# Optimization experiments

Measured on AMD Instinct MI355X. Metric: run time of the kernel, lower is better.

## Reference

```python
import jax, jax.numpy as jnp
import numpy as np

# static config (levels=4, CDA=False branch -> self_attn_4, scale=4, f=False)
SHAPES = [(80, 80), (40, 40), (20, 20), (10, 10)]
D = 256; NH = 8; NL = 4; NP = 4; DFF = 1024; DH = D // NH
L = sum(h * w for h, w in SHAPES)  # 8500
B = 1


def layer_norm(x, g, b, eps=1e-5):
    m = jnp.mean(x, axis=-1, keepdims=True)
    v = jnp.mean((x - m) ** 2, axis=-1, keepdims=True)
    return (x - m) * jax.lax.rsqrt(v + eps) * g + b


def ms_deform_attn_core(value, loc, attn):
    # value: [B, L, NH, DH]; loc: [B, Lq, NH, NL, NP, 2] in [0,1]; attn: [B, Lq, NH, NL, NP]
    Bq, Lq = loc.shape[0], loc.shape[1]
    out = jnp.zeros((Bq, NH, Lq, DH), value.dtype)
    start = 0
    for lvl, (Hl, Wl) in enumerate(SHAPES):
        v = value[:, start:start + Hl * Wl]          # [B, HW, NH, DH]
        start += Hl * Wl
        v = v.transpose(0, 2, 1, 3)                  # [B, NH, HW, DH]
        ll = loc[:, :, :, lvl]                       # [B, Lq, NH, NP, 2]
        # grid_sample semantics: align_corners=False, padding_mode='zeros'
        x = ll[..., 0] * Wl - 0.5
        y = ll[..., 1] * Hl - 0.5
        x0 = jnp.floor(x); y0 = jnp.floor(y)
        acc = jnp.zeros((Bq, NH, Lq, NP, DH), value.dtype)
        for dy in (0, 1):
            for dx in (0, 1):
                xi = x0 + dx; yi = y0 + dy
                w = (1.0 - jnp.abs(x - xi)) * (1.0 - jnp.abs(y - yi))  # [B,Lq,NH,NP]
                valid = (xi >= 0) & (xi < Wl) & (yi >= 0) & (yi < Hl)
                xi_c = jnp.clip(xi, 0, Wl - 1).astype(jnp.int32)
                yi_c = jnp.clip(yi, 0, Hl - 1).astype(jnp.int32)
                lin = (yi_c * Wl + xi_c).transpose(0, 2, 1, 3).reshape(Bq, NH, Lq * NP)
                g = jnp.take_along_axis(v, lin[..., None], axis=2).reshape(Bq, NH, Lq, NP, DH)
                wv = (w * valid.astype(w.dtype)).transpose(0, 2, 1, 3)[..., None]
                acc = acc + g * wv
        aw = attn[:, :, :, lvl].transpose(0, 2, 1, 3)[..., None]  # [B,NH,Lq,NP,1]
        out = out + jnp.sum(acc * aw, axis=3)
    return out.transpose(0, 2, 1, 3).reshape(Bq, Lq, NH * DH)


def setup_inputs():
    key = jax.random.key(0)
    ks = jax.random.split(key, 24)
    s = 0.02
    d = {}
    d['src'] = jax.random.normal(ks[0], (B, L, D), jnp.float32)
    d['pos'] = jax.random.normal(ks[1], (B, L, D), jnp.float32)
    d['reference_points'] = jax.random.uniform(ks[2], (B, L, NL, 2), jnp.float32)
    d['spatial_shapes'] = jnp.array(SHAPES, jnp.int32)
    d['level_start_index'] = jnp.array(np.cumsum([0] + [h * w for h, w in SHAPES[:-1]]), jnp.int32)
    d['scale'] = 4
    # MSDeformAttn params
    d['Wo'] = jax.random.normal(ks[3], (D, NH * NL * NP * 2), jnp.float32) * s
    d['bo'] = jax.random.normal(ks[4], (NH * NL * NP * 2,), jnp.float32) * s
    d['Wa'] = jax.random.normal(ks[5], (D, NH * NL * NP), jnp.float32) * s
    d['ba'] = jax.random.normal(ks[6], (NH * NL * NP,), jnp.float32) * s
    d['Wv'] = jax.random.normal(ks[7], (D, D), jnp.float32) * s
    d['bv'] = jnp.zeros((D,), jnp.float32)
    d['Wout'] = jax.random.normal(ks[8], (D, D), jnp.float32) * s
    d['bout'] = jnp.zeros((D,), jnp.float32)
    # FFN + LayerNorms
    d['W1'] = jax.random.normal(ks[9], (D, DFF), jnp.float32) * s
    d['b1'] = jnp.zeros((DFF,), jnp.float32)
    d['W2'] = jax.random.normal(ks[10], (DFF, D), jnp.float32) * s
    d['b2'] = jnp.zeros((D,), jnp.float32)
    d['g1'] = jnp.ones((D,), jnp.float32); d['be1'] = jnp.zeros((D,), jnp.float32)
    d['g2'] = jnp.ones((D,), jnp.float32); d['be2'] = jnp.zeros((D,), jnp.float32)
    return d


def reference(src, pos, reference_points, spatial_shapes, level_start_index, scale,
              Wo, bo, Wa, ba, Wv, bv, Wout, bout, W1, b1, W2, b2, g1, be1, g2, be2):
    Bq, Lq, _ = src.shape
    q = src + pos  # with_pos_embed
    # sampling offsets & attention weights (softmax over levels*points)
    off = (q @ Wo + bo).reshape(Bq, Lq, NH, NL, NP, 2)
    attn = jax.nn.softmax((q @ Wa + ba).reshape(Bq, Lq, NH, NL * NP), axis=-1)
    attn = attn.reshape(Bq, Lq, NH, NL, NP)
    value = (src @ Wv + bv).reshape(Bq, L, NH, DH)
    # offset normalizer is (W, H) per level
    normalizer = jnp.stack([spatial_shapes[:, 1], spatial_shapes[:, 0]], -1).astype(src.dtype)
    loc = reference_points[:, :, None, :, None, :] + off / normalizer[None, None, None, :, None, :]
    src2 = ms_deform_attn_core(value, loc, attn) @ Wout + bout
    # residual + norm1 (dropout = eval identity)
    x = layer_norm(src + src2, g1, be1)
    # FFN
    ffn = jax.nn.relu(x @ W1 + b1) @ W2 + b2
    x = layer_norm(x + ffn, g2, be2)
    return x
```

## Files before the change

### kernel.cpp

```cpp
#include <hip/hip_runtime.h>
#include <hip/hip_bf16.h>
#include <string.h>

#define D 256
#define NH 8
#define DH 32
#define NL 4
#define NP 4
#define DFF 1024
#define LTOT 8500

typedef __bf16 bf16x8 __attribute__((ext_vector_type(8)));
typedef float floatx4 __attribute__((ext_vector_type(4)));

__device__ inline unsigned bpack(float a, float b) {
    __hip_bfloat16 ha = __float2bfloat16(a), hb = __float2bfloat16(b);
    unsigned short ua, ub;
    memcpy(&ua, &ha, 2); memcpy(&ub, &hb, 2);
    return (unsigned)ua | ((unsigned)ub << 16);
}

__global__ void transpose_all(const float* W0, const float* W1_, const float* W2_,
                              const float* W3, const float* W4, const float* W5,
                              __hip_bfloat16* T0, __hip_bfloat16* T1, __hip_bfloat16* T2,
                              __hip_bfloat16* T3, __hip_bfloat16* T4, __hip_bfloat16* T5) {
    const int cum[7] = {0, 64, 96, 160, 224, 480, 736};
    int id = blockIdx.x;
    int mi = 0;
    while (id >= cum[mi + 1]) mi++;
    int lid = id - cum[mi];
    const float* W; __hip_bfloat16* T; int K, N;
    switch (mi) {
        case 0: W = W0; T = T0; K = 256;  N = 256;  break;
        case 1: W = W1_; T = T1; K = 256; N = 128;  break;
        case 2: W = W2_; T = T2; K = 256; N = 256;  break;
        case 3: W = W3; T = T3; K = 256;  N = 256;  break;
        case 4: W = W4; T = T4; K = 256;  N = 1024; break;
        default: W = W5; T = T5; K = 1024; N = 256; break;
    }
    int ntx = N >> 5;
    int n0 = (lid % ntx) * 32, k0 = (lid / ntx) * 32;
    __shared__ float t[32][33];
    int tx = threadIdx.x & 31, ty = threadIdx.x >> 5;
#pragma unroll
    for (int i = 0; i < 32; i += 8)
        t[ty + i][tx] = W[(size_t)(k0 + ty + i) * N + n0 + tx];
    __syncthreads();
#pragma unroll
    for (int i = 0; i < 32; i += 8)
        T[(size_t)(n0 + ty + i) * K + k0 + tx] = __float2bfloat16(t[tx][ty + i]);
}

template<int BM, int BN>
__global__ __launch_bounds__(256) void gemm_mfma(
    const __hip_bfloat16* __restrict__ A, const __hip_bfloat16* __restrict__ BT,
    const float* __restrict__ bias, float* __restrict__ Cf, __hip_bfloat16* __restrict__ Cb,
    int M, int N, int K, int relu) {
    constexpr int BK = 32;
    constexpr int LDA = BK + 8;
    __shared__ __align__(16) __hip_bfloat16 sA[BM * LDA];
    __shared__ __align__(16) __hip_bfloat16 sB[BN * LDA];

    int tid = threadIdx.x;
    int wave = tid >> 6, lane = tid & 63;
    int m0 = blockIdx.y * BM;
    int n0 = blockIdx.x * BN;
    constexpr int WM = BM / 2, WN = BN / 2;
    int wm = (wave >> 1) * WM;
    int wn = (wave & 1) * WN;
    constexpr int TM = WM / 16, TN = WN / 16;

    floatx4 acc[TM][TN];
#pragma unroll
    for (int i = 0; i < TM; i++)
#pragma unroll
        for (int j = 0; j < TN; j++)
#pragma unroll
            for (int e = 0; e < 4; e++) acc[i][j][e] = 0.f;

    constexpr int RA = BM / 64, RB = BN / 64;
    int rowT = tid >> 2;
    int c16 = tid & 3;
    int lrow = lane & 15;
    int lk = (lane >> 4) * 8;

    int growA[RA];
#pragma unroll
    for (int r = 0; r < RA; r++) {
        int g = m0 + r * 64 + rowT; if (g >= M) g = M - 1;
        growA[r] = g;
    }

    bf16x8 pa[RA], pb[RB];
#pragma unroll
    for (int r = 0; r < RA; r++)
        pa[r] = *(const bf16x8*)(A + (size_t)growA[r] * K + c16 * 8);
#pragma unroll
    for (int r = 0; r < RB; r++)
        pb[r] = *(const bf16x8*)(BT + (size_t)(n0 + r * 64 + rowT) * K + c16 * 8);

    for (int k0 = 0; k0 < K; k0 += BK) {
#pragma unroll
        for (int r = 0; r < RA; r++)
            *(bf16x8*)(&sA[(r * 64 + rowT) * LDA + c16 * 8]) = pa[r];
#pragma unroll
        for (int r = 0; r < RB; r++)
            *(bf16x8*)(&sB[(r * 64 + rowT) * LDA + c16 * 8]) = pb[r];
        __syncthreads();

        int kn = k0 + BK;
        if (kn < K) {
#pragma unroll
            for (int r = 0; r < RA; r++)
                pa[r] = *(const bf16x8*)(A + (size_t)growA[r] * K + kn + c16 * 8);
#pragma unroll
            for (int r = 0; r < RB; r++)
                pb[r] = *(const bf16x8*)(BT + (size_t)(n0 + r * 64 + rowT) * K + kn + c16 * 8);
        }

        bf16x8 af[TM], bfr[TN];
#pragma unroll
        for (int tm = 0; tm < TM; tm++)
            af[tm] = *(const bf16x8*)(&sA[(wm + tm * 16 + lrow) * LDA + lk]);
#pragma unroll
        for (int tn = 0; tn < TN; tn++)
            bfr[tn] = *(const bf16x8*)(&sB[(wn + tn * 16 + lrow) * LDA + lk]);
#pragma unroll
        for (int tm = 0; tm < TM; tm++)
#pragma unroll
            for (int tn = 0; tn < TN; tn++)
                acc[tm][tn] = __builtin_amdgcn_mfma_f32_16x16x32_bf16(af[tm], bfr[tn], acc[tm][tn], 0, 0, 0);
        __syncthreads();
    }

    int lcol = lane & 15;
    int lr4 = (lane >> 4) * 4;
#pragma unroll
    for (int tm = 0; tm < TM; tm++) {
#pragma unroll
        for (int i = 0; i < 4; i++) {
            int row = m0 + wm + tm * 16 + lr4 + i;
            if (row < M) {
#pragma unroll
                for (int tn = 0; tn < TN; tn++) {
                    int col = n0 + wn + tn * 16 + lcol;
                    float v = acc[tm][tn][i] + bias[col];
                    if (relu) v = fmaxf(v, 0.f);
                    if (Cf) Cf[(size_t)row * N + col] = v;
                    if (Cb) Cb[(size_t)row * N + col] = __float2bfloat16(v);
                }
            }
        }
    }
}

__global__ __launch_bounds__(256) void proj_fused(
    const float* __restrict__ src, const float* __restrict__ pos,
    const __hip_bfloat16* __restrict__ WoT, const __hip_bfloat16* __restrict__ WaT,
    const __hip_bfloat16* __restrict__ WvT,
    const float* __restrict__ bo, const float* __restrict__ ba, const float* __restrict__ bv,
    float* __restrict__ locb, float* __restrict__ attnb, __hip_bfloat16* __restrict__ valb,
    int M) {
    constexpr int BM = 64, BN = 128, BK = 32, K = 256;
    constexpr int LDA = BK + 8;
    __shared__ __align__(16) __hip_bfloat16 sA[BM * LDA];
    __shared__ __align__(16) __hip_bfloat16 sB[BN * LDA];

    int n0 = blockIdx.x * BN;
    int m0 = blockIdx.y * BM;

    const __hip_bfloat16* BT;
    const float* bias;
    int ncol0, Nout, usePos;
    float* Cf; __hip_bfloat16* Cb;
    if (n0 < 256)      { BT = WoT; bias = bo; ncol0 = n0;       Nout = 256; Cf = locb;  Cb = nullptr; usePos = 1; }
    else if (n0 < 384) { BT = WaT; bias = ba; ncol0 = n0 - 256; Nout = 128; Cf = attnb; Cb = nullptr; usePos = 1; }
    else               { BT = WvT; bias = bv; ncol0 = n0 - 384; Nout = 256; Cf = nullptr; Cb = valb; usePos = 0; }

    int tid = threadIdx.x;
    int wave = tid >> 6, lane = tid & 63;
    int wm = (wave >> 1) * 32;
    int wn = (wave & 1) * 64;

    floatx4 acc[2][4];
#pragma unroll
    for (int i = 0; i < 2; i++)
#pragma unroll
        for (int j = 0; j < 4; j++)
#pragma unroll
            for (int e = 0; e < 4; e++) acc[i][j][e] = 0.f;

    int rowT = tid >> 2, c16 = tid & 3;
    int lrow = lane & 15, lk = (lane >> 4) * 8;

    int growA = m0 + rowT; if (growA >= M) growA = M - 1;
    const float* aBase = src + (size_t)growA * K + c16 * 8;
    const float* pBase = pos + (size_t)growA * K + c16 * 8;

    float4 s0, s1, p0, p1;
    bf16x8 pb[2];
    {
        s0 = *(const float4*)aBase;
        s1 = *(const float4*)(aBase + 4);
        if (usePos) { p0 = *(const float4*)pBase; p1 = *(const float4*)(pBase + 4); }
#pragma unroll
        for (int r = 0; r < 2; r++)
            pb[r] = *(const bf16x8*)(BT + (size_t)(ncol0 + r * 64 + rowT) * K + c16 * 8);
    }

    for (int k0 = 0; k0 < K; k0 += BK) {
        {
            float4 a0 = s0, a1 = s1;
            if (usePos) {
                a0.x += p0.x; a0.y += p0.y; a0.z += p0.z; a0.w += p0.w;
                a1.x += p1.x; a1.y += p1.y; a1.z += p1.z; a1.w += p1.w;
            }
            uint4 pk;
            pk.x = bpack(a0.x, a0.y); pk.y = bpack(a0.z, a0.w);
            pk.z = bpack(a1.x, a1.y); pk.w = bpack(a1.z, a1.w);
            *(uint4*)(&sA[rowT * LDA + c16 * 8]) = pk;
#pragma unroll
            for (int r = 0; r < 2; r++)
                *(bf16x8*)(&sB[(r * 64 + rowT) * LDA + c16 * 8]) = pb[r];
        }
        __syncthreads();

        int kn = k0 + BK;
        if (kn < K) {
            s0 = *(const float4*)(aBase + kn);
            s1 = *(const float4*)(aBase + kn + 4);
            if (usePos) {
                p0 = *(const float4*)(pBase + kn);
                p1 = *(const float4*)(pBase + kn + 4);
            }
#pragma unroll
            for (int r = 0; r < 2; r++)
                pb[r] = *(const bf16x8*)(BT + (size_t)(ncol0 + r * 64 + rowT) * K + kn + c16 * 8);
        }

        bf16x8 af[2], bfr[4];
#pragma unroll
        for (int t = 0; t < 2; t++)
            af[t] = *(const bf16x8*)(&sA[(wm + t * 16 + lrow) * LDA + lk]);
#pragma unroll
        for (int t = 0; t < 4; t++)
            bfr[t] = *(const bf16x8*)(&sB[(wn + t * 16 + lrow) * LDA + lk]);
#pragma unroll
        for (int tm = 0; tm < 2; tm++)
#pragma unroll
            for (int tn = 0; tn < 4; tn++)
                acc[tm][tn] = __builtin_amdgcn_mfma_f32_16x16x32_bf16(af[tm], bfr[tn], acc[tm][tn], 0, 0, 0);
        __syncthreads();
    }

    int lcol = lane & 15, lr4 = (lane >> 4) * 4;
#pragma unroll
    for (int tm = 0; tm < 2; tm++) {
#pragma unroll
        for (int i = 0; i < 4; i++) {
            int row = m0 + wm + tm * 16 + lr4 + i;
            if (row < M) {
#pragma unroll
                for (int tn = 0; tn < 4; tn++) {
                    int col = ncol0 + wn + tn * 16 + lcol;
                    float v = acc[tm][tn][i] + bias[col];
                    if (Cf) Cf[(size_t)row * Nout + col] = v;
                    else    Cb[(size_t)row * Nout + col] = __float2bfloat16(v);
                }
            }
        }
    }
}

__global__ __launch_bounds__(256) void deform(const __hip_bfloat16* __restrict__ value,
                                              const float* __restrict__ locraw,
                                              const float* __restrict__ logits,
                                              const float* __restrict__ refp,
                                              __hip_bfloat16* __restrict__ out) {
    __shared__ float wS[4][8][16][4];
    __shared__ int   aS[4][8][16][4];
    int tid = threadIdx.x;
    int q0 = blockIdx.x * 4;

    {
        int sub = tid >> 6, h = (tid >> 3) & 7, t8 = tid & 7;
        int q = q0 + sub;
        const float* lg = logits + q * 128 + h * 16;
        float l0 = lg[t8], l1 = lg[t8 + 8];
        float mx = fmaxf(l0, l1);
#pragma unroll
        for (int m = 1; m < 8; m <<= 1) mx = fmaxf(mx, __shfl_xor(mx, m, 64));
        float e0 = __expf(l0 - mx), e1 = __expf(l1 - mx);
        float s = e0 + e1;
#pragma unroll
        for (int m = 1; m < 8; m <<= 1) s += __shfl_xor(s, m, 64);
        float inv = 1.f / s;

        const int starts[4] = {0, 6400, 8000, 8400};
#pragma unroll
        for (int j = 0; j < 2; j++) {
            int pp = t8 + 8 * j;
            float a = (j ? e1 : e0) * inv;
            int l = pp >> 2;
            int Wl = 80 >> l;
            float nv = (float)Wl;
            float rx = refp[q * 8 + l * 2 + 0];
            float ry = refp[q * 8 + l * 2 + 1];
            float lx = rx + locraw[q * 256 + h * 32 + pp * 2 + 0] / nv;
            float ly = ry + locraw[q * 256 + h * 32 + pp * 2 + 1] / nv;
            float x = lx * nv - 0.5f;
            float y = ly * nv - 0.5f;
            float x0f = floorf(x), y0f = floorf(y);
            float fx = x - x0f, fy = y - y0f;
            int x0 = (int)x0f, y0 = (int)y0f;
            float wts[4] = {(1.f - fx) * (1.f - fy), fx * (1.f - fy),
                            (1.f - fx) * fy,         fx * fy};
            int st = starts[l];
#pragma unroll
            for (int t = 0; t < 4; t++) {
                int xi = x0 + (t & 1), yi = y0 + (t >> 1);
                bool valid = (xi >= 0) & (xi < Wl) & (yi >= 0) & (yi < Wl);
                int xc = min(max(xi, 0), Wl - 1), yc = min(max(yi, 0), Wl - 1);
                wS[sub][h][pp][t] = valid ? wts[t] * a : 0.f;
                aS[sub][h][pp][t] = (st + yc * Wl + xc) * 512 + h * 64;
            }
        }
    }
    __syncthreads();

    int sub = tid >> 6, h = (tid >> 3) & 7, l8 = tid & 7;
    int q = q0 + sub;
    const char* vb = (const char*)value;
    int lo = l8 * 8;
    float a0 = 0.f, a1 = 0.f, a2 = 0.f, a3 = 0.f;
#pragma unroll
    for (int p = 0; p < 16; p++) {
        floatx4 w = *(const floatx4*)&wS[sub][h][p][0];
        int4 av = *(const int4*)&aS[sub][h][p][0];
#pragma unroll
        for (int t = 0; t < 4; t++) {
            int ad = (t == 0) ? av.x : (t == 1) ? av.y : (t == 2) ? av.z : av.w;
            uint2 u = *(const uint2*)(vb + ad + lo);
            float wt = w[t];
            a0 += wt * __uint_as_float(u.x << 16);
            a1 += wt * __uint_as_float(u.x & 0xffff0000u);
            a2 += wt * __uint_as_float(u.y << 16);
            a3 += wt * __uint_as_float(u.y & 0xffff0000u);
        }
    }
    uint2 o;
    o.x = bpack(a0, a1);
    o.y = bpack(a2, a3);
    *(uint2*)((char*)out + q * 512 + h * 64 + l8 * 8) = o;
}

__global__ __launch_bounds__(512) void gemm_ln(
    const __hip_bfloat16* __restrict__ A, const __hip_bfloat16* __restrict__ BT,
    const float* __restrict__ bias, const float* __restrict__ resid,
    const float* __restrict__ g, const float* __restrict__ be,
    float* __restrict__ outf, __hip_bfloat16* __restrict__ outb,
    int M, int K) {
    constexpr int BM = 32, BK = 32, LDA = BK + 8;
    __shared__ __align__(16) __hip_bfloat16 sA[BM * LDA];
    __shared__ __align__(16) __hip_bfloat16 sB[256 * LDA];
    __shared__ float psum[8][32], psq[8][32], mS[32], rS[32];

    int tid = threadIdx.x;
    int wave = tid >> 6, lane = tid & 63;
    int m0 = blockIdx.x * BM;

    floatx4 acc[2][2];
#pragma unroll
    for (int i = 0; i < 2; i++)
#pragma unroll
        for (int j = 0; j < 2; j++)
#pragma unroll
            for (int e = 0; e < 4; e++) acc[i][j][e] = 0.f;

    int rowT = tid >> 2, c16 = tid & 3;
    int lrow = lane & 15, lk = (lane >> 4) * 8;

    int growA = m0 + rowT; if (growA >= M) growA = M - 1;

    bf16x8 pA, pB[2];
    if (tid < 128)
        pA = *(const bf16x8*)(A + (size_t)growA * K + c16 * 8);
#pragma unroll
    for (int r = 0; r < 2; r++)
        pB[r] = *(const bf16x8*)(BT + (size_t)(r * 128 + rowT) * K + c16 * 8);

    for (int k0 = 0; k0 < K; k0 += BK) {
        if (tid < 128)
            *(bf16x8*)(&sA[rowT * LDA + c16 * 8]) = pA;
#pragma unroll
        for (int r = 0; r < 2; r++)
            *(bf16x8*)(&sB[(r * 128 + rowT) * LDA + c16 * 8]) = pB[r];
        __syncthreads();

        int kn = k0 + BK;
        if (kn < K) {
            if (tid < 128)
                pA = *(const bf16x8*)(A + (size_t)growA * K + kn + c16 * 8);
#pragma unroll
            for (int r = 0; r < 2; r++)
                pB[r] = *(const bf16x8*)(BT + (size_t)(r * 128 + rowT) * K + kn + c16 * 8);
        }

        bf16x8 af[2], bfr[2];
#pragma unroll
        for (int tm = 0; tm < 2; tm++)
            af[tm] = *(const bf16x8*)(&sA[(tm * 16 + lrow) * LDA + lk]);
#pragma unroll
        for (int tn = 0; tn < 2; tn++)
            bfr[tn] = *(const bf16x8*)(&sB[(wave * 32 + tn * 16 + lrow) * LDA + lk]);
#pragma unroll
        for (int tm = 0; tm < 2; tm++)
#pragma unroll
            for (int tn = 0; tn < 2; tn++)
                acc[tm][tn] = __builtin_amdgcn_mfma_f32_16x16x32_bf16(af[tm], bfr[tn], acc[tm][tn], 0, 0, 0);
        __syncthreads();
    }

    int lcol = lane & 15, quad = lane >> 4;
    float v[2][2][4];
#pragma unroll
    for (int tm = 0; tm < 2; tm++) {
#pragma unroll
        for (int i = 0; i < 4; i++) {
            int row = tm * 16 + quad * 4 + i;
            int grow = m0 + row; if (grow >= M) grow = M - 1;
#pragma unroll
            for (int tn = 0; tn < 2; tn++) {
                int col = wave * 32 + tn * 16 + lcol;
                v[tm][tn][i] = acc[tm][tn][i] + bias[col] + resid[(size_t)grow * 256 + col];
            }
        }
    }

#pragma unroll
    for (int tm = 0; tm < 2; tm++) {
#pragma unroll
        for (int i = 0; i < 4; i++) {
            float s = 0.f, s2 = 0.f;
#pragma unroll
            for (int tn = 0; tn < 2; tn++) { float x = v[tm][tn][i]; s += x; s2 += x * x; }
#pragma unroll
            for (int m = 1; m < 16; m <<= 1) {
                s  += __shfl_xor(s, m, 64);
                s2 += __shfl_xor(s2, m, 64);
            }
            if (lcol == 0) {
                int row = tm * 16 + quad * 4 + i;
                psum[wave][row] = s;
                psq[wave][row]  = s2;
            }
        }
    }
    __syncthreads();
    if (tid < 32) {
        float s = 0.f, s2 = 0.f;
#pragma unroll
        for (int w = 0; w < 8; w++) { s += psum[w][tid]; s2 += psq[w][tid]; }
        float m = s * (1.f / 256.f);
        float var = fmaxf(s2 * (1.f / 256.f) - m * m, 0.f);
        mS[tid] = m;
        rS[tid] = rsqrtf(var + 1e-5f);
    }
    __syncthreads();

#pragma unroll
    for (int tm = 0; tm < 2; tm++) {
#pragma unroll
        for (int i = 0; i < 4; i++) {
            int row = tm * 16 + quad * 4 + i;
            int grow = m0 + row;
            if (grow < M) {
                float m = mS[row], r = rS[row];
#pragma unroll
                for (int tn = 0; tn < 2; tn++) {
                    int col = wave * 32 + tn * 16 + lcol;
                    float o = (v[tm][tn][i] - m) * r * g[col] + be[col];
                    outf[(size_t)grow * 256 + col] = o;
                    if (outb) outb[(size_t)grow * 256 + col] = __float2bfloat16(o);
                }
            }
        }
    }
}

extern "C" void kernel_launch(void* const* d_in, const int* in_sizes, int n_in,
                              void* d_out, int out_size, void* d_ws, size_t ws_size,
                              hipStream_t stream) {
    const float* src  = (const float*)d_in[0];
    const float* pos  = (const float*)d_in[1];
    const float* refp = (const float*)d_in[2];
    const float* Wo   = (const float*)d_in[6];
    const float* bo   = (const float*)d_in[7];
    const float* Wa   = (const float*)d_in[8];
    const float* ba   = (const float*)d_in[9];
    const float* Wv   = (const float*)d_in[10];
    const float* bv   = (const float*)d_in[11];
    const float* Wout = (const float*)d_in[12];
    const float* bout = (const float*)d_in[13];
    const float* W1   = (const float*)d_in[14];
    const float* b1   = (const float*)d_in[15];
    const float* W2   = (const float*)d_in[16];
    const float* b2   = (const float*)d_in[17];
    const float* g1   = (const float*)d_in[18];
    const float* be1  = (const float*)d_in[19];
    const float* g2   = (const float*)d_in[20];
    const float* be2  = (const float*)d_in[21];
    float* out = (float*)d_out;
    char* ws = (char*)d_ws;

    __hip_bfloat16* WoT   = (__hip_bfloat16*)(ws + 0);
    __hip_bfloat16* WaT   = (__hip_bfloat16*)(ws + 131072);
    __hip_bfloat16* WvT   = (__hip_bfloat16*)(ws + 196608);
    __hip_bfloat16* WoutT = (__hip_bfloat16*)(ws + 327680);
    __hip_bfloat16* W1T   = (__hip_bfloat16*)(ws + 458752);
    __hip_bfloat16* W2T   = (__hip_bfloat16*)(ws + 983040);
    float*          locb  = (float*)(ws + 1507328);
    float*          attnb = (float*)(ws + 10211328);
    __hip_bfloat16* valb  = (__hip_bfloat16*)(ws + 14563328);
    __hip_bfloat16* aob   = (__hip_bfloat16*)(ws + 18915328);
    float*          x1    = (float*)(ws + 23267328);
    __hip_bfloat16* x1b   = (__hip_bfloat16*)(ws + 31971328);
    __hip_bfloat16* hb    = (__hip_bfloat16*)(ws + 36323328);

    transpose_all<<<736, 256, 0, stream>>>(Wo, Wa, Wv, Wout, W1, W2,
                                           WoT, WaT, WvT, WoutT, W1T, W2T);

    proj_fused<<<dim3(5, 133), 256, 0, stream>>>(src, pos, WoT, WaT, WvT, bo, ba, bv,
                                                 locb, attnb, valb, LTOT);

    deform<<<2125, 256, 0, stream>>>(valb, locb, attnb, refp, aob);

    gemm_ln<<<266, 512, 0, stream>>>(aob, WoutT, bout, src, g1, be1, x1, x1b, LTOT, 256);

    gemm_mfma<128, 128><<<dim3(8, 67), 256, 0, stream>>>(x1b, W1T, b1, nullptr, hb, LTOT, 1024, 256, 1);

    gemm_ln<<<266, 512, 0, stream>>>(hb, W2T, b2, x1, g2, be2, out, nullptr, LTOT, 1024);
}
```

Baseline: 207.7 us.

## Use direct global-to-LDS loads in GEMMs and pre-convert src/pos to bf16

Replaces the register-staged, padded LDS tile loads in all GEMM kernels with global_load_lds 16-byte direct copies into an unpadded layout. The copies are issued after the loop-top sync with no register prefetch of the next tile. The transpose kernel gains extra blocks that convert src and src+pos to bf16 once, so the projection GEMM reads bf16 directly and moves to 128x128 tiles. The aim is to cut VGPR staging and global traffic, at the cost of possible LDS bank conflicts from dropping the padding and less overlap of loads with MFMA work.

Result: slower. 212.7 us (+2.4%).

```diff
diff --git a/kernel.cpp b/kernel.cpp
--- a/kernel.cpp
+++ b/kernel.cpp
@@ -20,12 +20,37 @@
     return (unsigned)ua | ((unsigned)ub << 16);
 }
 
+__device__ inline void gload16(const void* g, void* l) {
+    __builtin_amdgcn_global_load_lds((const __attribute__((address_space(1))) void*)g,
+                                     (__attribute__((address_space(3))) void*)l,
+                                     16, 0, 0);
+}
+
 __global__ void transpose_all(const float* W0, const float* W1_, const float* W2_,
                               const float* W3, const float* W4, const float* W5,
                               __hip_bfloat16* T0, __hip_bfloat16* T1, __hip_bfloat16* T2,
-                              __hip_bfloat16* T3, __hip_bfloat16* T4, __hip_bfloat16* T5) {
+                              __hip_bfloat16* T3, __hip_bfloat16* T4, __hip_bfloat16* T5,
+                              const float* src, const float* pos,
+                              __hip_bfloat16* qb, __hip_bfloat16* srcb) {
+    int id = blockIdx.x;
+    if (id >= 736) {
+        int idx = (id - 736) * 2048 + threadIdx.x * 8;
+        if (idx < LTOT * 256) {
+            float4 s0 = *(const float4*)(src + idx);
+            float4 s1 = *(const float4*)(src + idx + 4);
+            float4 p0 = *(const float4*)(pos + idx);
+            float4 p1 = *(const float4*)(pos + idx + 4);
+            uint4 us, uq;
+            us.x = bpack(s0.x, s0.y); us.y = bpack(s0.z, s0.w);
+            us.z = bpack(s1.x, s1.y); us.w = bpack(s1.z, s1.w);
+            uq.x = bpack(s0.x + p0.x, s0.y + p0.y); uq.y = bpack(s0.z + p0.z, s0.w + p0.w);
+            uq.z = bpack(s1.x + p1.x, s1.y + p1.y); uq.w = bpack(s1.z + p1.z, s1.w + p1.w);
+            *(uint4*)(srcb + idx) = us;
+            *(uint4*)(qb + idx)  = uq;
+        }
+        return;
+    }
     const int cum[7] = {0, 64, 96, 160, 224, 480, 736};
-    int id = blockIdx.x;
     int mi = 0;
     while (id >= cum[mi + 1]) mi++;
     int lid = id - cum[mi];
@@ -51,98 +76,73 @@
         T[(size_t)(n0 + ty + i) * K + k0 + tx] = __float2bfloat16(t[tx][ty + i]);
 }
 
-template<int BM, int BN>
-__global__ __launch_bounds__(256) void gemm_mfma(
+__global__ __launch_bounds__(256) void gemm97(
     const __hip_bfloat16* __restrict__ A, const __hip_bfloat16* __restrict__ BT,
     const float* __restrict__ bias, float* __restrict__ Cf, __hip_bfloat16* __restrict__ Cb,
     int M, int N, int K, int relu) {
-    constexpr int BK = 32;
-    constexpr int LDA = BK + 8;
-    __shared__ __align__(16) __hip_bfloat16 sA[BM * LDA];
-    __shared__ __align__(16) __hip_bfloat16 sB[BN * LDA];
-
-    int tid = threadIdx.x;
-    int wave = tid >> 6, lane = tid & 63;
-    int m0 = blockIdx.y * BM;
-    int n0 = blockIdx.x * BN;
-    constexpr int WM = BM / 2, WN = BN / 2;
-    int wm = (wave >> 1) * WM;
-    int wn = (wave & 1) * WN;
-    constexpr int TM = WM / 16, TN = WN / 16;
-
-    floatx4 acc[TM][TN];
-#pragma unroll
-    for (int i = 0; i < TM; i++)
-#pragma unroll
-        for (int j = 0; j < TN; j++)
+    constexpr int BM = 128, BN = 128, BK = 32;
+    __shared__ __align__(16) __hip_bfloat16 sA[BM * BK];
+    __shared__ __align__(16) __hip_bfloat16 sB[BN * BK];
+
+    int tid = threadIdx.x, wave = tid >> 6, lane = tid & 63;
+    int m0 = blockIdx.y * BM, n0 = blockIdx.x * BN;
+    int wm = (wave >> 1) * 64, wn = (wave & 1) * 64;
+
+    floatx4 acc[4][4];
+#pragma unroll
+    for (int i = 0; i < 4; i++)
+#pragma unroll
+        for (int j = 0; j < 4; j++)
 #pragma unroll
             for (int e = 0; e < 4; e++) acc[i][j][e] = 0.f;
 
-    constexpr int RA = BM / 64, RB = BN / 64;
-    int rowT = tid >> 2;
-    int c16 = tid & 3;
-    int lrow = lane & 15;
-    int lk = (lane >> 4) * 8;
-
-    int growA[RA];
-#pragma unroll
-    for (int r = 0; r < RA; r++) {
-        int g = m0 + r * 64 + rowT; if (g >= M) g = M - 1;
-        growA[r] = g;
-    }
-
-    bf16x8 pa[RA], pb[RB];
-#pragma unroll
-    for (int r = 0; r < RA; r++)
-        pa[r] = *(const bf16x8*)(A + (size_t)growA[r] * K + c16 * 8);
-#pragma unroll
-    for (int r = 0; r < RB; r++)
-        pb[r] = *(const bf16x8*)(BT + (size_t)(n0 + r * 64 + rowT) * K + c16 * 8);
+    int l4r = lane >> 2;
+    int l4c = (lane & 3) * 8;
+    int lrow = lane & 15, lk = (lane >> 4) * 8;
+
+    int grA[2];
+#pragma unroll
+    for (int i = 0; i < 2; i++) {
+        int g = m0 + wave * 32 + i * 16 + l4r;
+        if (g >= M) g = M - 1;
+        grA[i] = g;
+    }
 
     for (int k0 = 0; k0 < K; k0 += BK) {
 #pragma unroll
-        for (int r = 0; r < RA; r++)
-            *(bf16x8*)(&sA[(r * 64 + rowT) * LDA + c16 * 8]) = pa[r];
-#pragma unroll
-        for (int r = 0; r < RB; r++)
-            *(bf16x8*)(&sB[(r * 64 + rowT) * LDA + c16 * 8]) = pb[r];
+        for (int i = 0; i < 2; i++)
+            gload16(A + (size_t)grA[i] * K + k0 + l4c,
+                    (char*)sA + wave * 2048 + i * 1024);
+#pragma unroll
+        for (int i = 0; i < 2; i++)
+            gload16(BT + (size_t)(n0 + wave * 32 + i * 16 + l4r) * K + k0 + l4c,
+                    (char*)sB + wave * 2048 + i * 1024);
         __syncthreads();
 
-        int kn = k0 + BK;
-        if (kn < K) {
-#pragma unroll
-            for (int r = 0; r < RA; r++)
-                pa[r] = *(const bf16x8*)(A + (size_t)growA[r] * K + kn + c16 * 8);
-#pragma unroll
-            for (int r = 0; r < RB; r++)
-                pb[r] = *(const bf16x8*)(BT + (size_t)(n0 + r * 64 + rowT) * K + kn + c16 * 8);
-        }
-
-        bf16x8 af[TM], bfr[TN];
-#pragma unroll
-        for (int tm = 0; tm < TM; tm++)
-            af[tm] = *(const bf16x8*)(&sA[(wm + tm * 16 + lrow) * LDA + lk]);
-#pragma unroll
-        for (int tn = 0; tn < TN; tn++)
-            bfr[tn] = *(const bf16x8*)(&sB[(wn + tn * 16 + lrow) * LDA + lk]);
-#pragma unroll
-        for (int tm = 0; tm < TM; tm++)
-#pragma unroll
-            for (int tn = 0; tn < TN; tn++)
+        bf16x8 af[4], bfr[4];
+#pragma unroll
+        for (int tm = 0; tm < 4; tm++)
+            af[tm] = *(const bf16x8*)(&sA[(wm + tm * 16 + lrow) * BK + lk]);
+#pragma unroll
+        for (int tn = 0; tn < 4; tn++)
+            bfr[tn] = *(const bf16x8*)(&sB[(wn + tn * 16 + lrow) * BK + lk]);
+#pragma unroll
+        for (int tm = 0; tm < 4; tm++)
+#pragma unroll
+            for (int tn = 0; tn < 4; tn++)
                 acc[tm][tn] = __builtin_amdgcn_mfma_f32_16x16x32_bf16(af[tm], bfr[tn], acc[tm][tn], 0, 0, 0);
         __syncthreads();
     }
 
-    int lcol = lane & 15;
-    int lr4 = (lane >> 4) * 4;
-#pragma unroll
-    for (int tm = 0; tm < TM; tm++) {
+    int lcol = lane & 15, lr4 = (lane >> 4) * 4;
+#pragma unroll
+    for (int tm = 0; tm < 4; tm++) {
 #pragma unroll
         for (int i = 0; i < 4; i++) {
             int row = m0 + wm + tm * 16 + lr4 + i;
             if (row < M) {
 #pragma unroll
-                for (int tn = 0; tn < TN; tn++) {
+                for (int tn = 0; tn < 4; tn++) {
                     int col = n0 + wn + tn * 16 + lcol;
                     float v = acc[tm][tn][i] + bias[col];
                     if (relu) v = fmaxf(v, 0.f);
@@ -154,99 +154,71 @@
     }
 }
 
-__global__ __launch_bounds__(256) void proj_fused(
-    const float* __restrict__ src, const float* __restrict__ pos,
+__global__ __launch_bounds__(256) void proj2(
+    const __hip_bfloat16* __restrict__ qb, const __hip_bfloat16* __restrict__ srcb,
     const __hip_bfloat16* __restrict__ WoT, const __hip_bfloat16* __restrict__ WaT,
     const __hip_bfloat16* __restrict__ WvT,
     const float* __restrict__ bo, const float* __restrict__ ba, const float* __restrict__ bv,
     float* __restrict__ locb, float* __restrict__ attnb, __hip_bfloat16* __restrict__ valb,
     int M) {
-    constexpr int BM = 64, BN = 128, BK = 32, K = 256;
-    constexpr int LDA = BK + 8;
-    __shared__ __align__(16) __hip_bfloat16 sA[BM * LDA];
-    __shared__ __align__(16) __hip_bfloat16 sB[BN * LDA];
+    constexpr int BM = 128, BN = 128, BK = 32, K = 256;
+    __shared__ __align__(16) __hip_bfloat16 sA[BM * BK];
+    __shared__ __align__(16) __hip_bfloat16 sB[BN * BK];
 
     int n0 = blockIdx.x * BN;
     int m0 = blockIdx.y * BM;
 
     const __hip_bfloat16* BT;
+    const __hip_bfloat16* A;
     const float* bias;
-    int ncol0, Nout, usePos;
+    int ncol0, Nout;
     float* Cf; __hip_bfloat16* Cb;
-    if (n0 < 256)      { BT = WoT; bias = bo; ncol0 = n0;       Nout = 256; Cf = locb;  Cb = nullptr; usePos = 1; }
-    else if (n0 < 384) { BT = WaT; bias = ba; ncol0 = n0 - 256; Nout = 128; Cf = attnb; Cb = nullptr; usePos = 1; }
-    else               { BT = WvT; bias = bv; ncol0 = n0 - 384; Nout = 256; Cf = nullptr; Cb = valb; usePos = 0; }
-
-    int tid = threadIdx.x;
-    int wave = tid >> 6, lane = tid & 63;
-    int wm = (wave >> 1) * 32;
-    int wn = (wave & 1) * 64;
-
-    floatx4 acc[2][4];
-#pragma unroll
-    for (int i = 0; i < 2; i++)
+    if (n0 < 256)      { A = qb;   BT = WoT; bias = bo; ncol0 = n0;       Nout = 256; Cf = locb;  Cb = nullptr; }
+    else if (n0 < 384) { A = qb;   BT = WaT; bias = ba; ncol0 = 0;        Nout = 128; Cf = attnb; Cb = nullptr; }
+    else               { A = srcb; BT = WvT; bias = bv; ncol0 = n0 - 384; Nout = 256; Cf = nullptr; Cb = valb; }
+
+    int tid = threadIdx.x, wave = tid >> 6, lane = tid & 63;
+    int wm = (wave >> 1) * 64, wn = (wave & 1) * 64;
+
+    floatx4 acc[4][4];
+#pragma unroll
+    for (int i = 0; i < 4; i++)
 #pragma unroll
         for (int j = 0; j < 4; j++)
 #pragma unroll
             for (int e = 0; e < 4; e++) acc[i][j][e] = 0.f;
 
-    int rowT = tid >> 2, c16 = tid & 3;
+    int l4r = lane >> 2, l4c = (lane & 3) * 8;
     int lrow = lane & 15, lk = (lane >> 4) * 8;
 
-    int growA = m0 + rowT; if (growA >= M) growA = M - 1;
-    const float* aBase = src + (size_t)growA * K + c16 * 8;
-    const float* pBase = pos + (size_t)growA * K + c16 * 8;
-
-    float4 s0, s1, p0, p1;
-    bf16x8 pb[2];
-    {
-        s0 = *(const float4*)aBase;
-        s1 = *(const float4*)(aBase + 4);
-        if (usePos) { p0 = *(const float4*)pBase; p1 = *(const float4*)(pBase + 4); }
-#pragma unroll
-        for (int r = 0; r < 2; r++)
-            pb[r] = *(const bf16x8*)(BT + (size_t)(ncol0 + r * 64 + rowT) * K + c16 * 8);
+    int grA[2];
+#pragma unroll
+    for (int i = 0; i < 2; i++) {
+        int g = m0 + wave * 32 + i * 16 + l4r;
+        if (g >= M) g = M - 1;
+        grA[i] = g;
     }
 
     for (int k0 = 0; k0 < K; k0 += BK) {
-        {
-            float4 a0 = s0, a1 = s1;
-            if (usePos) {
-                a0.x += p0.x; a0.y += p0.y; a0.z += p0.z; a0.w += p0.w;
-                a1.x += p1.x; a1.y += p1.y; a1.z += p1.z; a1.w += p1.w;
-            }
-            uint4 pk;
-            pk.x = bpack(a0.x, a0.y); pk.y = bpack(a0.z, a0.w);
-            pk.z = bpack(a1.x, a1.y); pk.w = bpack(a1.z, a1.w);
-            *(uint4*)(&sA[rowT * LDA + c16 * 8]) = pk;
-#pragma unroll
-            for (int r = 0; r < 2; r++)
-                *(bf16x8*)(&sB[(r * 64 + rowT) * LDA + c16 * 8]) = pb[r];
-        }
+#pragma unroll
+        for (int i = 0; i < 2; i++)
+            gload16(A + (size_t)grA[i] * K + k0 + l4c,
+                    (char*)sA + wave * 2048 + i * 1024);
+#pragma unroll
+        for (int i = 0; i < 2; i++)
+            gload16(BT + (size_t)(ncol0 + wave * 32 + i * 16 + l4r) * K + k0 + l4c,
+                    (char*)sB + wave * 2048 + i * 1024);
         __syncthreads();
 
-        int kn = k0 + BK;
-        if (kn < K) {
-            s0 = *(const float4*)(aBase + kn);
-            s1 = *(const float4*)(aBase + kn + 4);
-            if (usePos) {
-                p0 = *(const float4*)(pBase + kn);
-                p1 = *(const float4*)(pBase + kn + 4);
-            }
-#pragma unroll
-            for (int r = 0; r < 2; r++)
-                pb[r] = *(const bf16x8*)(BT + (size_t)(ncol0 + r * 64 + rowT) * K + kn + c16 * 8);
-        }
-
-        bf16x8 af[2], bfr[4];
-#pragma unroll
-        for (int t = 0; t < 2; t++)
-            af[t] = *(const bf16x8*)(&sA[(wm + t * 16 + lrow) * LDA + lk]);
-#pragma unroll
-        for (int t = 0; t < 4; t++)
-            bfr[t] = *(const bf16x8*)(&sB[(wn + t * 16 + lrow) * LDA + lk]);
-#pragma unroll
-        for (int tm = 0; tm < 2; tm++)
+        bf16x8 af[4], bfr[4];
+#pragma unroll
+        for (int tm = 0; tm < 4; tm++)
+            af[tm] = *(const bf16x8*)(&sA[(wm + tm * 16 + lrow) * BK + lk]);
+#pragma unroll
+        for (int tn = 0; tn < 4; tn++)
+            bfr[tn] = *(const bf16x8*)(&sB[(wn + tn * 16 + lrow) * BK + lk]);
+#pragma unroll
+        for (int tm = 0; tm < 4; tm++)
 #pragma unroll
             for (int tn = 0; tn < 4; tn++)
                 acc[tm][tn] = __builtin_amdgcn_mfma_f32_16x16x32_bf16(af[tm], bfr[tn], acc[tm][tn], 0, 0, 0);
@@ -255,7 +227,7 @@
 
     int lcol = lane & 15, lr4 = (lane >> 4) * 4;
 #pragma unroll
-    for (int tm = 0; tm < 2; tm++) {
+    for (int tm = 0; tm < 4; tm++) {
 #pragma unroll
         for (int i = 0; i < 4; i++) {
             int row = m0 + wm + tm * 16 + lr4 + i;
@@ -360,9 +332,9 @@
     const float* __restrict__ g, const float* __restrict__ be,
     float* __restrict__ outf, __hip_bfloat16* __restrict__ outb,
     int M, int K) {
-    constexpr int BM = 32, BK = 32, LDA = BK + 8;
-    __shared__ __align__(16) __hip_bfloat16 sA[BM * LDA];
-    __shared__ __align__(16) __hip_bfloat16 sB[256 * LDA];
+    constexpr int BM = 32, BK = 32;
+    __shared__ __align__(16) __hip_bfloat16 sA[BM * BK];
+    __shared__ __align__(16) __hip_bfloat16 sB[256 * BK];
     __shared__ float psum[8][32], psq[8][32], mS[32], rS[32];
 
     int tid = threadIdx.x;
@@ -377,42 +349,28 @@
 #pragma unroll
             for (int e = 0; e < 4; e++) acc[i][j][e] = 0.f;
 
-    int rowT = tid >> 2, c16 = tid & 3;
+    int l4r = lane >> 2, l4c = (lane & 3) * 8;
     int lrow = lane & 15, lk = (lane >> 4) * 8;
 
-    int growA = m0 + rowT; if (growA >= M) growA = M - 1;
-
-    bf16x8 pA, pB[2];
-    if (tid < 128)
-        pA = *(const bf16x8*)(A + (size_t)growA * K + c16 * 8);
-#pragma unroll
-    for (int r = 0; r < 2; r++)
-        pB[r] = *(const bf16x8*)(BT + (size_t)(r * 128 + rowT) * K + c16 * 8);
+    int grA = m0 + wave * 16 + l4r;
+    if (grA >= M) grA = M - 1;
 
     for (int k0 = 0; k0 < K; k0 += BK) {
-        if (tid < 128)
-            *(bf16x8*)(&sA[rowT * LDA + c16 * 8]) = pA;
-#pragma unroll
-        for (int r = 0; r < 2; r++)
-            *(bf16x8*)(&sB[(r * 128 + rowT) * LDA + c16 * 8]) = pB[r];
+        if (wave < 2)
+            gload16(A + (size_t)grA * K + k0 + l4c, (char*)sA + wave * 1024);
+#pragma unroll
+        for (int i = 0; i < 2; i++)
+            gload16(BT + (size_t)(wave * 32 + i * 16 + l4r) * K + k0 + l4c,
+                    (char*)sB + wave * 2048 + i * 1024);
         __syncthreads();
 
-        int kn = k0 + BK;
-        if (kn < K) {
-            if (tid < 128)
-                pA = *(const bf16x8*)(A + (size_t)growA * K + kn + c16 * 8);
-#pragma unroll
-            for (int r = 0; r < 2; r++)
-                pB[r] = *(const bf16x8*)(BT + (size_t)(r * 128 + rowT) * K + kn + c16 * 8);
-        }
-
         bf16x8 af[2], bfr[2];
 #pragma unroll
         for (int tm = 0; tm < 2; tm++)
-            af[tm] = *(const bf16x8*)(&sA[(tm * 16 + lrow) * LDA + lk]);
+            af[tm] = *(const bf16x8*)(&sA[(tm * 16 + lrow) * BK + lk]);
 #pragma unroll
         for (int tn = 0; tn < 2; tn++)
-            bfr[tn] = *(const bf16x8*)(&sB[(wave * 32 + tn * 16 + lrow) * LDA + lk]);
+            bfr[tn] = *(const bf16x8*)(&sB[(wave * 32 + tn * 16 + lrow) * BK + lk]);
 #pragma unroll
         for (int tm = 0; tm < 2; tm++)
 #pragma unroll
@@ -526,18 +484,21 @@
     float*          x1    = (float*)(ws + 23267328);
     __hip_bfloat16* x1b   = (__hip_bfloat16*)(ws + 31971328);
     __hip_bfloat16* hb    = (__hip_bfloat16*)(ws + 36323328);
-
-    transpose_all<<<736, 256, 0, stream>>>(Wo, Wa, Wv, Wout, W1, W2,
-                                           WoT, WaT, WvT, WoutT, W1T, W2T);
-
-    proj_fused<<<dim3(5, 133), 256, 0, stream>>>(src, pos, WoT, WaT, WvT, bo, ba, bv,
-                                                 locb, attnb, valb, LTOT);
+    __hip_bfloat16* qb    = (__hip_bfloat16*)(ws + 36323328);
+    __hip_bfloat16* srcb  = (__hip_bfloat16*)(ws + 36323328 + 4352000);
+
+    transpose_all<<<736 + 1063, 256, 0, stream>>>(Wo, Wa, Wv, Wout, W1, W2,
+                                                  WoT, WaT, WvT, WoutT, W1T, W2T,
+                                                  src, pos, qb, srcb);
+
+    proj2<<<dim3(5, 67), 256, 0, stream>>>(qb, srcb, WoT, WaT, WvT, bo, ba, bv,
+                                           locb, attnb, valb, LTOT);
 
     deform<<<2125, 256, 0, stream>>>(valb, locb, attnb, refp, aob);
 
     gemm_ln<<<266, 512, 0, stream>>>(aob, WoutT, bout, src, g1, be1, x1, x1b, LTOT, 256);
 
-    gemm_mfma<128, 128><<<dim3(8, 67), 256, 0, stream>>>(x1b, W1T, b1, nullptr, hb, LTOT, 1024, 256, 1);
+    gemm97<<<dim3(8, 67), 256, 0, stream>>>(x1b, W1T, b1, nullptr, hb, LTOT, 1024, 256, 1);
 
     gemm_ln<<<266, 512, 0, stream>>>(hb, W2T, b2, x1, g2, be2, out, nullptr, LTOT, 1024);
 }
```
